# Performance work log

Measured on AMD Instinct MI355X. Metric: run time of the kernel, lower is better.

Reference implementation:

```python
import jax, jax.numpy as jnp
import numpy as np

B, N, D, K = 4, 4096, 128, 20

def setup_inputs() -> dict:
    key = jax.random.key(0)
    k1, k2, k3 = jax.random.split(key, 3)
    s = 1.0 / np.sqrt(D)
    return {
        "x": jax.random.normal(k1, (B, N, D), dtype=jnp.float32),
        "Wq": jax.random.normal(k2, (D, D), dtype=jnp.float32) * s,
        "bq": jnp.zeros((D,), dtype=jnp.float32),
        "Wk": jax.random.normal(k3, (D, D), dtype=jnp.float32) * s,
        "bk": jnp.zeros((D,), dtype=jnp.float32),
    }

def reference(x, Wq, bq, Wk, bk):
    # Q/K projections: [B,N,D]
    Q = jnp.einsum('bnd,de->bne', x, Wq) + bq
    Kp = jnp.einsum('bnd,de->bne', x, Wk) + bk
    # scores: [B,N,N], scaled by sqrt(D)
    attn = jnp.einsum('bnd,bmd->bnm', Q, Kp) / jnp.sqrt(jnp.float32(D))
    # top-k along last dim -> binary mask via scatter
    _, topk_idx = jax.lax.top_k(attn, K)  # [B,N,K]
    bi = jnp.arange(B)[:, None, None]
    ni = jnp.arange(N)[None, :, None]
    mask = jnp.zeros_like(attn).at[bi, ni, topk_idx].set(1.0)
    # zero out non-topk entries, then full softmax over all N (zeros included,
    # matching the torch module exactly)
    sparse_attn = attn * mask
    out = jax.nn.softmax(sparse_attn, axis=-1)
    return out[..., None]  # [B,N,N,1]
```

## Files before the change

kernel.cpp:

```cpp
#include <hip/hip_runtime.h>

#define BN 4096
#define BD 128
#define NB 4
#define TOPK 20
#define CAND 96
#define EPS_U 0.9f

typedef float f32x16 __attribute__((ext_vector_type(16)));
typedef short bf16x8 __attribute__((ext_vector_type(8)));

__device__ inline unsigned short f2bf(float f) {
  unsigned int u = __float_as_uint(f);
  unsigned int r = (u + 0x7FFFu + ((u >> 16) & 1u)) >> 16;
  return (unsigned short)r;
}

__global__ __launch_bounds__(256) void proj_kernel(
    const float* __restrict__ x,
    const float* __restrict__ Wq, const float* __restrict__ bq,
    const float* __restrict__ Wk, const float* __restrict__ bk,
    double* __restrict__ Qd, double* __restrict__ Kd, unsigned short* __restrict__ Khi) {
  __shared__ double xs[32][129];
  const int tid = threadIdx.x;
  const long row0 = (long)blockIdx.x * 32;
  const float* xsrc = x + row0 * BD;
  for (int i = tid; i < 32 * BD; i += 256) xs[i >> 7][i & 127] = (double)xsrc[i];
  __syncthreads();

  const int e = tid & 127;
  const bool isK = tid >= 128;
  const float* W = isK ? Wk : Wq;
  const float* bias = isK ? bk : bq;
  double* Od = isK ? Kd : Qd;

  double acc[32];
  const double binit = (double)bias[e];
#pragma unroll
  for (int r = 0; r < 32; ++r) acc[r] = binit;

  for (int d = 0; d < BD; ++d) {
    const double wv = (double)W[d * BD + e];
#pragma unroll
    for (int r = 0; r < 32; ++r) acc[r] = fma(xs[r][d], wv, acc[r]);
  }

#pragma unroll
  for (int r = 0; r < 32; ++r) {
    const double a = acc[r];
    const long o = (row0 + r) * BD + e;
    Od[o] = a;
    if (isK) Khi[o] = f2bf((float)a);
  }
}

__global__ __launch_bounds__(512) void screen_kernel(
    const double* __restrict__ Qd, const unsigned short* __restrict__ Khi,
    unsigned short* __restrict__ Sbf) {
  __shared__ char sbuf[8][2560];

  const int tid = threadIdx.x;
  const int lane = tid & 63;
  const int w = tid >> 6;
  const int kt = w & 3, qt = w >> 2;
  const int c31 = lane & 31, hi = lane >> 5;

  const int blk = blockIdx.x;
  const int xcd = blk & 7;
  const int j = blk >> 3;
  const int combo = xcd * 2 + (j & 1);
  const int b = combo >> 2;
  const int kq = combo & 3;
  const int rg = j >> 1;
  const int rowbase = rg << 6;
  const int kvbase = kq << 10;

  const int qrow = qt * 32 + c31;
  const long grow = (long)b * BN + rowbase + qrow;

  bf16x8 bqf[8];
  {
    const double* qp = Qd + grow * BD + hi * 8;
#pragma unroll
    for (int ks = 0; ks < 8; ++ks) {
      bf16x8 pk;
#pragma unroll
      for (int jj = 0; jj < 8; ++jj) pk[jj] = (short)f2bf((float)qp[ks * 16 + jj]);
      bqf[ks] = pk;
    }
  }

  const unsigned short* kb = Khi + ((long)b * BN + kvbase + kt * 32 + c31) * BD + hi * 8;
  char* my = sbuf[w];
  const int wr = c31 * 80;

  const long gq = (long)b * BN + rowbase + qt * 32 + (lane >> 1);
  unsigned short* dstbase = Sbf + gq * BN + kvbase + kt * 32 + (lane & 1) * 16;
  const char* rdp = my + (lane >> 1) * 80 + (lane & 1) * 32;

  for (int step = 0; step < 8; ++step) {
    const unsigned short* kr = kb + (long)step * 128 * BD;
    f32x16 acc = {0.f, 0.f, 0.f, 0.f, 0.f, 0.f, 0.f, 0.f,
                  0.f, 0.f, 0.f, 0.f, 0.f, 0.f, 0.f, 0.f};
#pragma unroll
    for (int ks = 0; ks < 8; ++ks) {
      const bf16x8 a = *(const bf16x8*)(kr + ks * 16);
      acc = __builtin_amdgcn_mfma_f32_32x32x16_bf16(a, bqf[ks], acc, 0, 0, 0);
    }

#pragma unroll
    for (int p = 0; p < 4; ++p) {
      const unsigned int lo =
          (unsigned int)f2bf(acc[p * 4 + 0]) | ((unsigned int)f2bf(acc[p * 4 + 1]) << 16);
      const unsigned int hi2 =
          (unsigned int)f2bf(acc[p * 4 + 2]) | ((unsigned int)f2bf(acc[p * 4 + 3]) << 16);
      *(uint2*)(my + wr + p * 16 + hi * 8) = make_uint2(lo, hi2);
    }
    const uint4 r0 = *(const uint4*)(rdp);
    const uint4 r1 = *(const uint4*)(rdp + 16);
    unsigned short* dst = dstbase + step * 128;
    *(uint4*)dst = r0;
    *(uint4*)(dst + 8) = r1;
  }
}

__device__ inline float rescore_f64(const double2* __restrict__ kp2, const double2* __restrict__ q2) {
  double a0 = 0.0, a1 = 0.0, a2 = 0.0, a3 = 0.0;
#pragma unroll
  for (int i = 0; i < 64; i += 4) {
    a0 = fma(q2[i + 0].y, kp2[i + 0].y, fma(q2[i + 0].x, kp2[i + 0].x, a0));
    a1 = fma(q2[i + 1].y, kp2[i + 1].y, fma(q2[i + 1].x, kp2[i + 1].x, a1));
    a2 = fma(q2[i + 2].y, kp2[i + 2].y, fma(q2[i + 2].x, kp2[i + 2].x, a2));
    a3 = fma(q2[i + 3].y, kp2[i + 3].y, fma(q2[i + 3].x, kp2[i + 3].x, a3));
  }
  return (float)(((a0 + a1) + (a2 + a3)) * 8.8388347648318447e-02);
}

__device__ inline unsigned int fmono(float v) {
  const unsigned int u = __float_as_uint(v);
  return (u & 0x80000000u) ? ~u : (u | 0x80000000u);
}
__device__ inline float fdemono(unsigned int k) {
  const unsigned int u = (k & 0x80000000u) ? (k & 0x7fffffffu) : ~k;
  return __uint_as_float(u);
}

__global__ __launch_bounds__(256) void topkfill_kernel(
    const double* __restrict__ Qd, const double* __restrict__ Kd,
    const unsigned short* __restrict__ Sbf, float* __restrict__ out) {
  __shared__ unsigned short listL[4][CAND];
  __shared__ unsigned int cntL[4];
  __shared__ unsigned int bm[4][128];
  __shared__ float pvL[4][TOPK];
  __shared__ int pcL[4][TOPK];

  const int tid = threadIdx.x;
  const int lane = tid & 63;
  const int w = tid >> 6;
  const int blk = blockIdx.x;
  const int b = (blk & 7) >> 1;
  const int idx = ((blk >> 3) << 1) | (blk & 1);
  const long row = (long)b * BN + idx * 4 + w;

  const unsigned short* srow = Sbf + row * BN;

  uint4 v[8];
  float pm[8];
#pragma unroll
  for (int i = 0; i < 8; ++i) {
    v[i] = *(const uint4*)(srow + i * 512 + lane * 8);
    float m0 = -3.4e38f;
#pragma unroll
    for (int k = 0; k < 4; ++k) {
      const unsigned int u = (&v[i].x)[k];
      m0 = fmaxf(m0, fmaxf(__uint_as_float(u << 16), __uint_as_float(u & 0xFFFF0000u)));
    }
    pm[i] = m0;
  }
  float mymax = fmaxf(fmaxf(fmaxf(pm[0], pm[1]), fmaxf(pm[2], pm[3])),
                      fmaxf(fmaxf(pm[4], pm[5]), fmaxf(pm[6], pm[7])));

  float vb = mymax;
#pragma unroll
  for (int k = 2; k <= 64; k <<= 1) {
#pragma unroll
    for (int jj = k >> 1; jj > 0; jj >>= 1) {
      const float o = __shfl_xor(vb, jj);
      const bool keepmin = (((lane & k) == 0) == ((lane & jj) == 0));
      vb = keepmin ? fminf(vb, o) : fmaxf(vb, o);
    }
  }
  const float th = __shfl(vb, 44) - EPS_U;

  if (lane == 0) cntL[w] = 0;
  bm[w][lane] = 0;
  bm[w][lane + 64] = 0;

#pragma unroll
  for (int i = 0; i < 8; ++i) {
#pragma unroll
    for (int k = 0; k < 4; ++k) {
      const unsigned int u = (&v[i].x)[k];
      const float f0 = __uint_as_float(u << 16);
      const float f1 = __uint_as_float(u & 0xFFFF0000u);
      const int col0 = i * 512 + lane * 8 + k * 2;
      if (f0 >= th) {
        const unsigned int p = atomicAdd(&cntL[w], 1u);
        if (p < CAND) listL[w][p] = (unsigned short)col0;
      }
      if (f1 >= th) {
        const unsigned int p = atomicAdd(&cntL[w], 1u);
        if (p < CAND) listL[w][p] = (unsigned short)(col0 + 1);
      }
    }
  }

  const int c = (int)min(cntL[w], (unsigned int)CAND);

  const double2* q2 = (const double2*)(Qd + row * BD);
  const double* kbd = Kd + (long)b * BN * BD;

  unsigned long long key0 = 0ull, key1 = 0ull;
  if (lane < c) {
    const int kv = (int)listL[w][lane];
    const float vv = rescore_f64((const double2*)(kbd + (long)kv * BD), q2);
    key0 = ((unsigned long long)fmono(vv) << 12) | (unsigned int)(4095 - kv);
  }
  if (lane + 64 < c) {
    const int kv = (int)listL[w][lane + 64];
    const float vv = rescore_f64((const double2*)(kbd + (long)kv * BD), q2);
    key1 = ((unsigned long long)fmono(vv) << 12) | (unsigned int)(4095 - kv);
  }
  if (key1 > key0) { const unsigned long long t = key0; key0 = key1; key1 = t; }

  float m = 0.0f, se = 0.0f;
  float myval = 0.0f;
  int mycol = 0;
  for (int it = 0; it < TOPK; ++it) {
    unsigned long long rk = key0;
    for (int off = 32; off; off >>= 1) {
      const unsigned long long ok = __shfl_xor(rk, off);
      rk = (ok > rk) ? ok : rk;
    }
    const float rv = fdemono((unsigned int)(rk >> 12));
    if (it == 0) m = fmaxf(rv, 0.0f);
    se += expf(rv - m);
    if (lane == it) { myval = rv; mycol = 4095 - (int)(rk & 0xFFFull); }
    if (key0 == rk) { key0 = key1; key1 = 0ull; }
  }

  const float Z = se + (float)(BN - TOPK) * expf(-m);
  const float c0 = expf(-m) / Z;

  if (lane < TOPK) {
    pvL[w][lane] = expf(myval - m) / Z;
    pcL[w][lane] = mycol;
    atomicOr(&bm[w][mycol >> 5], 1u << (mycol & 31));
  }

  const float4 cv = make_float4(c0, c0, c0, c0);
  float4* op = (float4*)(out + row * BN);
#pragma unroll
  for (int i = 0; i < 16; ++i) {
    const int j = i * 64 + lane;
    const unsigned int bits = (bm[w][j >> 3] >> ((j & 7) * 4)) & 0xFu;
    if (bits == 0u) {
      op[j] = cv;
    } else {
      float4 vv = cv;
      const int colb = j * 4;
#pragma unroll
      for (int cmp = 0; cmp < 4; ++cmp) {
        if ((bits >> cmp) & 1u) {
          const int col = colb + cmp;
          float pvv = c0;
          for (int t = 0; t < TOPK; ++t)
            if (pcL[w][t] == col) pvv = pvL[w][t];
          (&vv.x)[cmp] = pvv;
        }
      }
      op[j] = vv;
    }
  }
}

extern "C" void kernel_launch(void* const* d_in, const int* in_sizes, int n_in,
                              void* d_out, int out_size, void* d_ws, size_t ws_size,
                              hipStream_t stream) {
  const float* x  = (const float*)d_in[0];
  const float* Wq = (const float*)d_in[1];
  const float* bq = (const float*)d_in[2];
  const float* Wk = (const float*)d_in[3];
  const float* bk = (const float*)d_in[4];
  float* out = (float*)d_out;

  const long NE = (long)NB * BN * BD;
  double* Qd = (double*)d_ws;
  double* Kd = Qd + NE;
  unsigned short* Khi = (unsigned short*)(Kd + NE);
  unsigned short* Sbf = Khi + NE;

  proj_kernel<<<NB * BN / 32, 256, 0, stream>>>(x, Wq, bq, Wk, bk, Qd, Kd, Khi);
  screen_kernel<<<1024, 512, 0, stream>>>(Qd, Khi, Sbf);
  topkfill_kernel<<<NB * BN / 4, 256, 0, stream>>>(Qd, Kd, Sbf, out);
}
```

Before: 360.1 us.

## Split top-k selection from output fill and use bitonic sort for small candidate sets

```diff
diff --git a/kernel.cpp b/kernel.cpp
--- a/kernel.cpp
+++ b/kernel.cpp
@@ -145,14 +145,11 @@
   return __uint_as_float(u);
 }
 
-__global__ __launch_bounds__(256) void topkfill_kernel(
+__global__ __launch_bounds__(256) void topk_kernel(
     const double* __restrict__ Qd, const double* __restrict__ Kd,
-    const unsigned short* __restrict__ Sbf, float* __restrict__ out) {
+    const unsigned short* __restrict__ Sbf, unsigned int* __restrict__ rec) {
   __shared__ unsigned short listL[4][CAND];
   __shared__ unsigned int cntL[4];
-  __shared__ unsigned int bm[4][128];
-  __shared__ float pvL[4][TOPK];
-  __shared__ int pcL[4][TOPK];
 
   const int tid = threadIdx.x;
   const int lane = tid & 63;
@@ -193,8 +190,6 @@
   const float th = __shfl(vb, 44) - EPS_U;
 
   if (lane == 0) cntL[w] = 0;
-  bm[w][lane] = 0;
-  bm[w][lane + 64] = 0;
 
 #pragma unroll
   for (int i = 0; i < 8; ++i) {
@@ -231,55 +226,107 @@
     const float vv = rescore_f64((const double2*)(kbd + (long)kv * BD), q2);
     key1 = ((unsigned long long)fmono(vv) << 12) | (unsigned int)(4095 - kv);
   }
-  if (key1 > key0) { const unsigned long long t = key0; key0 = key1; key1 = t; }
-
-  float m = 0.0f, se = 0.0f;
-  float myval = 0.0f;
-  int mycol = 0;
-  for (int it = 0; it < TOPK; ++it) {
-    unsigned long long rk = key0;
-    for (int off = 32; off; off >>= 1) {
-      const unsigned long long ok = __shfl_xor(rk, off);
-      rk = (ok > rk) ? ok : rk;
-    }
-    const float rv = fdemono((unsigned int)(rk >> 12));
-    if (it == 0) m = fmaxf(rv, 0.0f);
-    se += expf(rv - m);
-    if (lane == it) { myval = rv; mycol = 4095 - (int)(rk & 0xFFFull); }
-    if (key0 == rk) { key0 = key1; key1 = 0ull; }
-  }
-
-  const float Z = se + (float)(BN - TOPK) * expf(-m);
-  const float c0 = expf(-m) / Z;
-
-  if (lane < TOPK) {
-    pvL[w][lane] = expf(myval - m) / Z;
-    pcL[w][lane] = mycol;
-    atomicOr(&bm[w][mycol >> 5], 1u << (mycol & 31));
-  }
-
+
+  unsigned int* rr = rec + row * 48;
+
+  if (c <= 64) {
+    unsigned long long kk = key0;
+#pragma unroll
+    for (int k = 2; k <= 64; k <<= 1) {
+#pragma unroll
+      for (int jj = k >> 1; jj > 0; jj >>= 1) {
+        const unsigned long long o = __shfl_xor(kk, jj);
+        const bool keepmin = (((lane & k) == 0) == ((lane & jj) == 0));
+        kk = keepmin ? (o < kk ? o : kk) : (o > kk ? o : kk);
+      }
+    }
+    const unsigned long long ktop = __shfl(kk, 63);
+    const float m = fmaxf(fdemono((unsigned int)(ktop >> 12)), 0.0f);
+    const float val = fdemono((unsigned int)(kk >> 12));
+    const int col = 4095 - (int)(kk & 0xFFFull);
+    const float e = (lane >= 44) ? expf(val - m) : 0.0f;
+    float se = e;
+#pragma unroll
+    for (int off = 32; off; off >>= 1) se += __shfl_xor(se, off);
+    const float Z = se + (float)(BN - TOPK) * expf(-m);
+    if (lane >= 44) {
+      const int r = 63 - lane;
+      rr[r] = __float_as_uint(e / Z);
+      rr[20 + r] = (unsigned int)col;
+    }
+    if (lane == 0) rr[40] = __float_as_uint(expf(-m) / Z);
+  } else {
+    if (key1 > key0) { const unsigned long long t = key0; key0 = key1; key1 = t; }
+    float m = 0.0f, se = 0.0f;
+    float myval = 0.0f;
+    int mycol = 0;
+    for (int it = 0; it < TOPK; ++it) {
+      unsigned long long rk = key0;
+      for (int off = 32; off; off >>= 1) {
+        const unsigned long long ok = __shfl_xor(rk, off);
+        rk = (ok > rk) ? ok : rk;
+      }
+      const float rv = fdemono((unsigned int)(rk >> 12));
+      if (it == 0) m = fmaxf(rv, 0.0f);
+      se += expf(rv - m);
+      if (lane == it) { myval = rv; mycol = 4095 - (int)(rk & 0xFFFull); }
+      if (key0 == rk) { key0 = key1; key1 = 0ull; }
+    }
+    const float Z = se + (float)(BN - TOPK) * expf(-m);
+    if (lane < TOPK) {
+      rr[lane] = __float_as_uint(expf(myval - m) / Z);
+      rr[20 + lane] = (unsigned int)mycol;
+    }
+    if (lane == 0) rr[40] = __float_as_uint(expf(-m) / Z);
+  }
+}
+
+__global__ __launch_bounds__(256) void fill_kernel(
+    const unsigned int* __restrict__ rec, float* __restrict__ out) {
+  __shared__ unsigned int bm[128];
+  __shared__ float pv[TOPK];
+  __shared__ int pc[TOPK];
+  __shared__ float sc0;
+
+  const int tid = threadIdx.x;
+  const long row = blockIdx.x;
+  const unsigned int* rr = rec + row * 48;
+
+  if (tid < 128) bm[tid] = 0;
+  __syncthreads();
+  if (tid < TOPK) {
+    pv[tid] = __uint_as_float(rr[tid]);
+    const int col = (int)rr[20 + tid];
+    pc[tid] = col;
+    atomicOr(&bm[col >> 5], 1u << (col & 31));
+  }
+  if (tid == TOPK) sc0 = __uint_as_float(rr[40]);
+  __syncthreads();
+
+  const float c0 = sc0;
   const float4 cv = make_float4(c0, c0, c0, c0);
   float4* op = (float4*)(out + row * BN);
-#pragma unroll
-  for (int i = 0; i < 16; ++i) {
-    const int j = i * 64 + lane;
-    const unsigned int bits = (bm[w][j >> 3] >> ((j & 7) * 4)) & 0xFu;
+
+#pragma unroll
+  for (int k = 0; k < 4; ++k) {
+    const int j = tid + k * 256;
+    const unsigned int bits = (bm[j >> 3] >> ((j & 7) * 4)) & 0xFu;
     if (bits == 0u) {
       op[j] = cv;
     } else {
-      float4 vv = cv;
-      const int colb = j * 4;
+      float4 v = cv;
+      const int col0 = j * 4;
 #pragma unroll
       for (int cmp = 0; cmp < 4; ++cmp) {
         if ((bits >> cmp) & 1u) {
-          const int col = colb + cmp;
+          const int col = col0 + cmp;
           float pvv = c0;
-          for (int t = 0; t < TOPK; ++t)
-            if (pcL[w][t] == col) pvv = pvL[w][t];
-          (&vv.x)[cmp] = pvv;
+          for (int i = 0; i < TOPK; ++i)
+            if (pc[i] == col) pvv = pv[i];
+          (&v.x)[cmp] = pvv;
         }
       }
-      op[j] = vv;
+      op[j] = v;
     }
   }
 }
@@ -295,12 +342,15 @@
   float* out = (float*)d_out;
 
   const long NE = (long)NB * BN * BD;
+  const long NR = (long)NB * BN;
   double* Qd = (double*)d_ws;
   double* Kd = Qd + NE;
   unsigned short* Khi = (unsigned short*)(Kd + NE);
   unsigned short* Sbf = Khi + NE;
+  unsigned int* rec = (unsigned int*)(Sbf + NR * BN);
 
   proj_kernel<<<NB * BN / 32, 256, 0, stream>>>(x, Wq, bq, Wk, bk, Qd, Kd, Khi);
   screen_kernel<<<1024, 512, 0, stream>>>(Qd, Khi, Sbf);
-  topkfill_kernel<<<NB * BN / 4, 256, 0, stream>>>(Qd, Kd, Sbf, out);
-}
+  topk_kernel<<<NR / 4, 256, 0, stream>>>(Qd, Kd, Sbf, rec);
+  fill_kernel<<<NR, 256, 0, stream>>>(rec, out);
+}
```

Result: faster. 326.0 us (-9.5%).
